# Performance work log

Measured on AMD Instinct MI355X. Metric: run time of the kernel, lower is better.

Reference implementation:

```python
import jax, jax.numpy as jnp
import numpy as np

N, M, C, IN, OUT = 65536, 512, 512, 256, 256
EPS = 1e-8


def setup_inputs() -> dict:
    key = jax.random.key(0)
    ks = jax.random.split(key, 12)
    d = {}
    d["x"] = jax.random.normal(ks[0], (1, IN), jnp.float32)
    d["memory"] = jax.random.normal(ks[1], (1, N, M), jnp.float32) * 0.05
    d["prev_read"] = jax.random.normal(ks[2], (1, M), jnp.float32) * 0.05
    d["h"] = jnp.ones((1, C), jnp.float32)
    d["c"] = jnp.ones((1, C), jnp.float32)
    d["read_state"] = jnp.zeros((1, N), jnp.float32)
    d["write_state"] = jnp.zeros((1, N), jnp.float32)
    d["W_ih"] = jax.random.normal(ks[3], (4 * C, IN + M), jnp.float32) * 0.02
    d["b_ih"] = jax.random.normal(ks[4], (4 * C,), jnp.float32) * 0.01
    d["W_hh"] = jax.random.normal(ks[5], (4 * C, C), jnp.float32) * 0.02
    d["b_hh"] = jax.random.normal(ks[6], (4 * C,), jnp.float32) * 0.01
    d["W_read"] = jax.random.normal(ks[7], (M + 6, C), jnp.float32) * 0.02
    d["b_read"] = jnp.zeros((M + 6,), jnp.float32)
    d["W_write"] = jax.random.normal(ks[8], (3 * M + 6, C), jnp.float32) * 0.02
    d["b_write"] = jnp.zeros((3 * M + 6,), jnp.float32)
    d["W_out"] = jax.random.normal(ks[9], (OUT, C + M), jnp.float32) * 0.02
    d["b_out"] = jnp.zeros((OUT,), jnp.float32)
    return d


def _address(head_out, w_prev, memory):
    # head_out: [B, M+6(+...)]; returns sharpened addressing weights [B, N]
    key_v = head_out[:, :M]
    beta = jax.nn.softplus(head_out[:, M:M + 1])          # [B,1]
    g = jax.nn.sigmoid(head_out[:, M + 1:M + 2])          # [B,1]
    shift = jax.nn.softmax(head_out[:, M + 2:M + 5], axis=1)  # [B,3]
    gamma = 1.0 + jax.nn.softplus(head_out[:, M + 5:M + 6])   # [B,1]
    # content addressing: cosine similarity over memory rows
    a = memory + EPS                                      # [B,N,M]
    b = key_v[:, None, :] + EPS                           # [B,1,M]
    dot = jnp.sum(a * b, axis=-1)                         # [B,N]
    na = jnp.maximum(jnp.sqrt(jnp.sum(a * a, axis=-1)), EPS)
    nb = jnp.maximum(jnp.sqrt(jnp.sum(b * b, axis=-1)), EPS)
    cos = dot / (na * nb)
    w_context = jax.nn.softmax(beta * cos, axis=1)        # [B,N]
    # NOTE: original code swaps args -> g gates the PREVIOUS weights
    w_interp = g * w_prev + (1.0 - g) * w_context
    # circular shift via 3-tap correlation (conv1d with circular pad)
    w_pad = jnp.concatenate([w_interp[:, -1:], w_interp, w_interp[:, :1]], axis=1)
    w_shift = (w_pad[:, :-2] * shift[:, 0:1]
               + w_pad[:, 1:-1] * shift[:, 1:2]
               + w_pad[:, 2:] * shift[:, 2:3])
    power = w_shift ** gamma
    return power / (jnp.sum(power, axis=1, keepdims=True) + EPS)


def reference(x, memory, prev_read, h, c, read_state, write_state,
              W_ih, b_ih, W_hh, b_hh, W_read, b_read, W_write, b_write,
              W_out, b_out):
    # LSTMCell controller (torch gate order: i, f, g, o)
    inp = jnp.concatenate([x, prev_read], axis=1)                   # [B, IN+M]
    gates = inp @ W_ih.T + b_ih + h @ W_hh.T + b_hh                 # [B, 4C]
    i_g, f_g, g_g, o_g = jnp.split(gates, 4, axis=1)
    c_new = jax.nn.sigmoid(f_g) * c + jax.nn.sigmoid(i_g) * jnp.tanh(g_g)
    h_new = jax.nn.sigmoid(o_g) * jnp.tanh(c_new)

    # read head
    r_out = h_new @ W_read.T + b_read
    w_r = _address(r_out, read_state, memory)                       # [B,N]
    # faithful to torch.matmul([B,N],[B,N,M]).sum(1): sums weights over batch
    read = jnp.einsum('n,bnm->bm', jnp.sum(w_r, axis=0), memory)    # [B,M]

    # write head
    w_out_head = h_new @ W_write.T + b_write
    w_w = _address(w_out_head, write_state, memory)                 # [B,N]
    erase = jax.nn.sigmoid(w_out_head[:, M + 6:2 * M + 6])          # [B,M]
    add = w_out_head[:, 2 * M + 6:3 * M + 6]                        # [B,M]
    memory_new = memory * (1.0 - w_w[:, :, None] * erase[:, None, :]) \
                 + w_w[:, :, None] * add[:, None, :]                # [B,N,M]

    out = jax.nn.sigmoid(jnp.concatenate([h_new, read], axis=1) @ W_out.T + b_out)
    del memory_new  # state update; torch forward returns only the output
    return out
```

## Files before the change

kernel.cpp:

```cpp
#include <hip/hip_runtime.h>
#include <math.h>

#define EPS 1e-8f
#define NN 65536
#define MAGIC 1.0f

#define WS_GATES 0
#define WS_HNEW  2048
#define WS_ROUT  2560
#define WS_PMAX  3104
#define WS_PEXP  5152
#define WS_S     7200
#define WS_PART  72992
#define WS_FLAGG 204064
#define WS_FLAGP 204192
#define WS_PART2 204448
#define WS_FLAG2 220832
#define WS_BF    262144
#define WS_PARTB 17039360
#define WS_PSUMB 18087936

typedef float f32x2 __attribute__((ext_vector_type(2)));

__device__ __forceinline__ float wave_sum(float v) {
    for (int o = 32; o > 0; o >>= 1) v += __shfl_xor(v, o);
    return v;
}
__device__ __forceinline__ float sigm(float x) { return 1.f / (1.f + expf(-x)); }
__device__ __forceinline__ float softplusf_(float x) {
    return x > 20.f ? x : log1pf(expf(x));
}
__device__ __forceinline__ float dot4(float4 a, float4 b) {
    return a.x * b.x + a.y * b.y + a.z * b.z + a.w * b.w;
}
__device__ __forceinline__ float4 ld4(const float* p) { return *(const float4*)p; }

__device__ __forceinline__ float ald(const float* p) {
    return __hip_atomic_load(p, __ATOMIC_RELAXED, __HIP_MEMORY_SCOPE_AGENT);
}
__device__ __forceinline__ void ast(float* p, float v) {
    __hip_atomic_store(p, v, __ATOMIC_RELAXED, __HIP_MEMORY_SCOPE_AGENT);
}
__device__ __forceinline__ void ast_rel(float* p, float v) {
    __hip_atomic_store(p, v, __ATOMIC_RELEASE, __HIP_MEMORY_SCOPE_AGENT);
}
__device__ __forceinline__ void acq_fence() {
    __builtin_amdgcn_fence(__ATOMIC_ACQUIRE, "agent");
}

__device__ __forceinline__ unsigned pk8(float4 v) {
    int u = __builtin_amdgcn_cvt_pk_fp8_f32(v.x, v.y, 0, false);
    u = __builtin_amdgcn_cvt_pk_fp8_f32(v.z, v.w, u, true);
    return (unsigned)u;
}

__global__ __launch_bounds__(256) void k_front(const float* __restrict__ x,
                                               const float* __restrict__ pr,
                                               const float* __restrict__ h,
                                               const float* __restrict__ c,
                                               const float* __restrict__ W_ih,
                                               const float* __restrict__ b_ih,
                                               const float* __restrict__ W_hh,
                                               const float* __restrict__ b_hh,
                                               const float* __restrict__ W_read,
                                               const float* __restrict__ b_read,
                                               float* __restrict__ ws) {
    const int b = blockIdx.x, t = threadIdx.x;
    const int lane = t & 63, wv = t >> 6;
    __shared__ float sh[512];

    if (b < 128) {
        #pragma unroll
        for (int i = 0; i < 4; ++i) {
            const int row = b * 16 + wv * 4 + i;
            const float* wi = W_ih + (size_t)row * 768;
            const float* wh = W_hh + (size_t)row * 512;
            float acc = dot4(ld4(wi + lane * 4), ld4(x + lane * 4))
                      + dot4(ld4(wi + 256 + lane * 4), ld4(pr + lane * 4))
                      + dot4(ld4(wi + 512 + lane * 4), ld4(pr + 256 + lane * 4))
                      + dot4(ld4(wh + lane * 4), ld4(h + lane * 4))
                      + dot4(ld4(wh + 256 + lane * 4), ld4(h + 256 + lane * 4));
            acc = wave_sum(acc);
            if (lane == 0) ast(ws + WS_GATES + row, acc + b_ih[row] + b_hh[row]);
        }
        __syncthreads();
        if (t == 0) ast_rel(ws + WS_FLAGG + b, MAGIC);
    }

    if (wv == 0) {
        int cap = 0;
        for (;;) {
            float v0 = ald(ws + WS_FLAGG + lane);
            float v1 = ald(ws + WS_FLAGG + 64 + lane);
            if (__all(v0 == MAGIC && v1 == MAGIC)) break;
            __builtin_amdgcn_s_sleep(1);
            if (++cap > (1 << 20)) break;
        }
        acq_fence();
    }
    __syncthreads();

    for (int j = t; j < 512; j += 256) {
        float ig = ald(ws + WS_GATES + j);
        float fg = ald(ws + WS_GATES + 512 + j);
        float gg = ald(ws + WS_GATES + 1024 + j);
        float og = ald(ws + WS_GATES + 1536 + j);
        float cn = sigm(fg) * c[j] + sigm(ig) * tanhf(gg);
        float hn = sigm(og) * tanhf(cn);
        sh[j] = hn;
        if (b == 0) ws[WS_HNEW + j] = hn;
    }
    __syncthreads();
    const int o = b * 4 + wv;
    if (o < 518) {
        const float* wr = W_read + (size_t)o * 512;
        float acc = dot4(ld4(wr + lane * 4), ld4(sh + lane * 4))
                  + dot4(ld4(wr + 256 + lane * 4), ld4(sh + 256 + lane * 4));
        acc = wave_sum(acc);
        if (lane == 0) ws[WS_ROUT + o] = acc + b_read[o];
    }
}

__global__ __launch_bounds__(256) void k_cos(const float* __restrict__ mem,
                                             float* __restrict__ ws) {
    const int t = threadIdx.x, lane = t & 63, wv = t >> 6;
    const int gw = blockIdx.x * 4 + wv;
    const float* key = ws + WS_ROUT;
    unsigned char* wsb = (unsigned char*)(ws + WS_BF);
    float4 ka = ld4(key + lane * 4);
    float4 kb = ld4(key + 256 + lane * 4);
    ka.x += EPS; ka.y += EPS; ka.z += EPS; ka.w += EPS;
    kb.x += EPS; kb.y += EPS; kb.z += EPS; kb.w += EPS;
    const float nb = fmaxf(__builtin_amdgcn_sqrtf(
                        wave_sum(dot4(ka, ka) + dot4(kb, kb))), EPS);
    const float beta = softplusf_(key[512]);
    float* sp = ws + WS_S;

    float4 va[4], vb[4], xa[4], xb[4];
    #pragma unroll
    for (int i = 0; i < 4; ++i) {
        const size_t n = (size_t)gw + i * 8192;
        va[i] = ld4(mem + n * 512 + lane * 4);
        vb[i] = ld4(mem + n * 512 + 256 + lane * 4);
    }
    #pragma unroll
    for (int i = 0; i < 4; ++i) {
        const size_t n = (size_t)gw + (4 + i) * 8192;
        xa[i] = ld4(mem + n * 512 + lane * 4);
        xb[i] = ld4(mem + n * 512 + 256 + lane * 4);
    }

    float m = -1e30f, e = 0.f;
    #pragma unroll
    for (int grp = 0; grp < 2; ++grp) {
        float d[4], q[4];
        #pragma unroll
        for (int i = 0; i < 4; ++i) {
            const size_t n = (size_t)gw + (grp * 4 + i) * 8192;
            *(unsigned*)(wsb + n * 512 + lane * 4) = pk8(va[i]);
            *(unsigned*)(wsb + n * 512 + 256 + lane * 4) = pk8(vb[i]);
            float4 wa = va[i], wb = vb[i];
            wa.x += EPS; wa.y += EPS; wa.z += EPS; wa.w += EPS;
            wb.x += EPS; wb.y += EPS; wb.z += EPS; wb.w += EPS;
            d[i] = dot4(wa, ka) + dot4(wb, kb);
            q[i] = dot4(wa, wa) + dot4(wb, wb);
        }
        if (grp == 0) {
            #pragma unroll
            for (int i = 0; i < 4; ++i) { va[i] = xa[i]; vb[i] = xb[i]; }
        }
        #pragma unroll
        for (int o = 32; o > 0; o >>= 1) {
            #pragma unroll
            for (int i = 0; i < 4; ++i) {
                d[i] += __shfl_xor(d[i], o);
                q[i] += __shfl_xor(q[i], o);
            }
        }
        float sv[4];
        #pragma unroll
        for (int i = 0; i < 4; ++i) {
            float na = fmaxf(__builtin_amdgcn_sqrtf(q[i]), EPS);
            sv[i] = beta * d[i] * __builtin_amdgcn_rcpf(na * nb);
        }
        float mysv = sv[0];
        if (lane == 1) mysv = sv[1];
        if (lane == 2) mysv = sv[2];
        if (lane == 3) mysv = sv[3];
        if (lane < 4) sp[gw + (grp * 4 + lane) * 8192] = mysv;
        float gm = fmaxf(fmaxf(sv[0], sv[1]), fmaxf(sv[2], sv[3]));
        float nm = fmaxf(m, gm);
        e = e * __expf(m - nm) + __expf(sv[0] - nm) + __expf(sv[1] - nm)
          + __expf(sv[2] - nm) + __expf(sv[3] - nm);
        m = nm;
    }

    __shared__ float sm[4], se[4];
    if (lane == 0) { sm[wv] = m; se[wv] = e; }
    __syncthreads();
    if (t == 0) {
        float M = fmaxf(fmaxf(sm[0], sm[1]), fmaxf(sm[2], sm[3]));
        float E = se[0] * __expf(sm[0] - M) + se[1] * __expf(sm[1] - M) +
                  se[2] * __expf(sm[2] - M) + se[3] * __expf(sm[3] - M);
        ws[WS_PMAX + blockIdx.x] = M;
        ws[WS_PEXP + blockIdx.x] = E;
    }
}

__global__ __launch_bounds__(256) void k_read(const float* __restrict__ rs,
                                              float* __restrict__ ws) {
    const int bb = blockIdx.x, t = threadIdx.x;
    const int lane = t & 63, wv = t >> 6;
    __shared__ float s_m[4], s_e[4];
    __shared__ float wi_l[34];
    __shared__ float pl[32];
    __shared__ float sacc[3][512];

    float m = -1e30f, e = 0.f;
    #pragma unroll
    for (int i = 0; i < 8; ++i) {
        float bm = ws[WS_PMAX + t + 256 * i], be = ws[WS_PEXP + t + 256 * i];
        float nm = fmaxf(m, bm);
        e = e * __expf(m - nm) + be * __expf(bm - nm);
        m = nm;
    }
    for (int o = 32; o > 0; o >>= 1) {
        float om = __shfl_xor(m, o), oe = __shfl_xor(e, o);
        float nm = fmaxf(m, om);
        e = e * __expf(m - nm) + oe * __expf(om - nm);
        m = nm;
    }
    if (lane == 0) { s_m[wv] = m; s_e[wv] = e; }
    __syncthreads();
    const float mx = fmaxf(fmaxf(s_m[0], s_m[1]), fmaxf(s_m[2], s_m[3]));
    const float Z = s_e[0] * __expf(s_m[0] - mx) + s_e[1] * __expf(s_m[1] - mx)
                  + s_e[2] * __expf(s_m[2] - mx) + s_e[3] * __expf(s_m[3] - mx);
    const float invZ = 1.f / Z;
    const float g = sigm(ws[WS_ROUT + 513]);
    float a3 = ws[WS_ROUT + 514], b3 = ws[WS_ROUT + 515], c3 = ws[WS_ROUT + 516];
    float mm = fmaxf(a3, fmaxf(b3, c3));
    float ea = __expf(a3 - mm), eb = __expf(b3 - mm), ec = __expf(c3 - mm);
    float ss = ea + eb + ec;
    const float s0 = ea / ss, s1 = eb / ss, s2 = ec / ss;
    const float gamma = 1.f + softplusf_(ws[WS_ROUT + 517]);

    const int start = bb * 32;
    if (t < 34) {
        int idx = (start - 1 + t) & (NN - 1);
        wi_l[t] = g * rs[idx] + (1.f - g) * __expf(ws[WS_S + idx] - mx) * invZ;
    }
    __syncthreads();
    float ps = 0.f;
    if (t < 32) {
        float wsh = wi_l[t] * s0 + wi_l[t + 1] * s1 + wi_l[t + 2] * s2;
        float pv = __powf(wsh, gamma);
        pl[t] = pv;
        ps = pv;
    }
    ps = wave_sum(ps);
    if (t == 0) ws[WS_PSUMB + bb] = ps;
    __syncthreads();

    const unsigned char* slab =
        (const unsigned char*)(ws + WS_BF) + (size_t)(start + wv * 8) * 512;
    float a0 = 0.f, a1 = 0.f, a2 = 0.f, a3f = 0.f,
          a4 = 0.f, a5 = 0.f, a6 = 0.f, a7 = 0.f;
    #pragma unroll
    for (int r = 0; r < 8; ++r) {
        float w = pl[wv * 8 + r];
        uint2 q = *(const uint2*)(slab + (size_t)r * 512 + lane * 8);
        f32x2 f0 = __builtin_amdgcn_cvt_pk_f32_fp8(q.x, false);
        f32x2 f1 = __builtin_amdgcn_cvt_pk_f32_fp8(q.x, true);
        f32x2 f2 = __builtin_amdgcn_cvt_pk_f32_fp8(q.y, false);
        f32x2 f3 = __builtin_amdgcn_cvt_pk_f32_fp8(q.y, true);
        a0 += w * f0.x;  a1 += w * f0.y;
        a2 += w * f1.x;  a3f += w * f1.y;
        a4 += w * f2.x;  a5 += w * f2.y;
        a6 += w * f3.x;  a7 += w * f3.y;
    }
    if (wv) {
        float* sw = sacc[wv - 1];
        sw[0 * 64 + lane] = a0; sw[1 * 64 + lane] = a1;
        sw[2 * 64 + lane] = a2; sw[3 * 64 + lane] = a3f;
        sw[4 * 64 + lane] = a4; sw[5 * 64 + lane] = a5;
        sw[6 * 64 + lane] = a6; sw[7 * 64 + lane] = a7;
    }
    __syncthreads();
    if (!wv) {
        #pragma unroll
        for (int i = 0; i < 3; ++i) {
            const float* sw = sacc[i];
            a0 += sw[0 * 64 + lane]; a1 += sw[1 * 64 + lane];
            a2 += sw[2 * 64 + lane]; a3f += sw[3 * 64 + lane];
            a4 += sw[4 * 64 + lane]; a5 += sw[5 * 64 + lane];
            a6 += sw[6 * 64 + lane]; a7 += sw[7 * 64 + lane];
        }
        float* pp = ws + WS_PARTB + (size_t)bb * 512 + lane * 8;
        *(float4*)pp = make_float4(a0, a1, a2, a3f);
        *(float4*)(pp + 4) = make_float4(a4, a5, a6, a7);
    }
}

__global__ __launch_bounds__(512) void k_out(const float* __restrict__ W_out,
                                             const float* __restrict__ b_out,
                                             float* __restrict__ ws,
                                             float* __restrict__ out) {
    const int b = blockIdx.x, t = threadIdx.x;
    const int lane = t & 63, wv = t >> 6;
    __shared__ float rd[512];
    __shared__ float s_z[8];

    {
        float s = 0.f;
        #pragma unroll
        for (int r = 0; r < 8; ++r)
            s += ws[WS_PARTB + (size_t)(8 * b + r) * 512 + t];
        ws[WS_PART + (size_t)b * 512 + t] = s;
    }
    __syncthreads();
    if (t == 0) ast_rel(ws + WS_FLAGP + b, MAGIC);
    if (b >= 32) return;

    if (wv == 0) {
        int cap = 0;
        for (;;) {
            float v0 = ald(ws + WS_FLAGP + lane);
            float v1 = ald(ws + WS_FLAGP + 64 + lane);
            float v2 = ald(ws + WS_FLAGP + 128 + lane);
            float v3 = ald(ws + WS_FLAGP + 192 + lane);
            if (__all(v0 == MAGIC && v1 == MAGIC && v2 == MAGIC && v3 == MAGIC))
                break;
            __builtin_amdgcn_s_sleep(1);
            if (++cap > (1 << 20)) break;
        }
        acq_fence();
    }
    __syncthreads();
    {
        float s = 0.f;
        #pragma unroll
        for (int r = 0; r < 8; ++r)
            s += ws[WS_PART + (size_t)(8 * b + r) * 512 + t];
        ws[WS_PART2 + (size_t)b * 512 + t] = s;
    }
    __syncthreads();
    if (t == 0) ast_rel(ws + WS_FLAG2 + b, MAGIC);
    if (wv == 0) {
        int cap = 0;
        for (;;) {
            float v = ald(ws + WS_FLAG2 + (lane & 31));
            if (__all(v == MAGIC)) break;
            __builtin_amdgcn_s_sleep(1);
            if (++cap > (1 << 20)) break;
        }
        acq_fence();
    }
    __syncthreads();
    float z = 0.f;
    #pragma unroll
    for (int i = 0; i < 4; ++i) z += ws[WS_PSUMB + t + 512 * i];
    z = wave_sum(z);
    if (lane == 0) s_z[wv] = z;
    __syncthreads();
    float Zp = 0.f;
    for (int i = 0; i < 8; ++i) Zp += s_z[i];
    const float invZp = 1.f / (Zp + EPS);
    {
        float s = 0.f;
        #pragma unroll
        for (int r = 0; r < 32; ++r)
            s += ws[WS_PART2 + (size_t)r * 512 + t];
        rd[t] = s * invZp;
    }
    __syncthreads();
    const int o = b * 8 + wv;
    const float* wo = W_out + (size_t)o * 1024;
    float a = dot4(ld4(wo + lane * 4), ld4(ws + WS_HNEW + lane * 4))
            + dot4(ld4(wo + 256 + lane * 4), ld4(ws + WS_HNEW + 256 + lane * 4))
            + dot4(ld4(wo + 512 + lane * 4), ld4(rd + lane * 4))
            + dot4(ld4(wo + 768 + lane * 4), ld4(rd + 256 + lane * 4));
    a = wave_sum(a);
    if (lane == 0) out[o] = sigm(a + b_out[o]);
}

extern "C" void kernel_launch(void* const* d_in, const int* in_sizes, int n_in,
                              void* d_out, int out_size, void* d_ws, size_t ws_size,
                              hipStream_t stream) {
    const float* x          = (const float*)d_in[0];
    const float* memory     = (const float*)d_in[1];
    const float* prev_read  = (const float*)d_in[2];
    const float* h          = (const float*)d_in[3];
    const float* c          = (const float*)d_in[4];
    const float* read_state = (const float*)d_in[5];
    const float* W_ih   = (const float*)d_in[7];
    const float* b_ih   = (const float*)d_in[8];
    const float* W_hh   = (const float*)d_in[9];
    const float* b_hh   = (const float*)d_in[10];
    const float* W_read = (const float*)d_in[11];
    const float* b_read = (const float*)d_in[12];
    const float* W_out  = (const float*)d_in[15];
    const float* b_out  = (const float*)d_in[16];
    float* ws  = (float*)d_ws;
    float* out = (float*)d_out;

    k_front<<<130, 256, 0, stream>>>(x, prev_read, h, c, W_ih, b_ih, W_hh, b_hh,
                                     W_read, b_read, ws);
    k_cos<<<2048, 256, 0, stream>>>(memory, ws);
    k_read<<<2048, 256, 0, stream>>>(read_state, ws);
    k_out<<<256, 512, 0, stream>>>(W_out, b_out, ws, out);
}
```

Measured before the change: 65.14 us.

## Fuse front LSTM/read-head kernel into cosine kernel with flag-based grid sync

Merges the front kernel (gates, LSTM cell, read-head projection) into the cosine-similarity kernel, launched as one 2048-block grid. The first 130 blocks do the front work and publish completion flags, and every block spins on those flags before the memory scan. This removes a kernel launch and its drain/fill gap. It also lets the memory loads be issued while earlier blocks finish. The cost is that the spin-wait relies on the first 130 blocks being scheduled and making progress, and the flags are never reset between calls.

```diff
diff --git a/kernel.cpp b/kernel.cpp
--- a/kernel.cpp
+++ b/kernel.cpp
@@ -16,6 +16,7 @@
 #define WS_FLAGP 204192
 #define WS_PART2 204448
 #define WS_FLAG2 220832
+#define WS_FLAGR 220864
 #define WS_BF    262144
 #define WS_PARTB 17039360
 #define WS_PSUMB 18087936
@@ -54,17 +55,18 @@
     return (unsigned)u;
 }
 
-__global__ __launch_bounds__(256) void k_front(const float* __restrict__ x,
-                                               const float* __restrict__ pr,
-                                               const float* __restrict__ h,
-                                               const float* __restrict__ c,
-                                               const float* __restrict__ W_ih,
-                                               const float* __restrict__ b_ih,
-                                               const float* __restrict__ W_hh,
-                                               const float* __restrict__ b_hh,
-                                               const float* __restrict__ W_read,
-                                               const float* __restrict__ b_read,
-                                               float* __restrict__ ws) {
+__global__ __launch_bounds__(256) void k_fc(const float* __restrict__ x,
+                                            const float* __restrict__ pr,
+                                            const float* __restrict__ h,
+                                            const float* __restrict__ c,
+                                            const float* __restrict__ W_ih,
+                                            const float* __restrict__ b_ih,
+                                            const float* __restrict__ W_hh,
+                                            const float* __restrict__ b_hh,
+                                            const float* __restrict__ W_read,
+                                            const float* __restrict__ b_read,
+                                            const float* __restrict__ mem,
+                                            float* __restrict__ ws) {
     const int b = blockIdx.x, t = threadIdx.x;
     const int lane = t & 63, wv = t >> 6;
     __shared__ float sh[512];
@@ -87,12 +89,49 @@
         if (t == 0) ast_rel(ws + WS_FLAGG + b, MAGIC);
     }
 
+    if (b < 130) {
+        if (wv == 0) {
+            int cap = 0;
+            for (;;) {
+                float v0 = ald(ws + WS_FLAGG + lane);
+                float v1 = ald(ws + WS_FLAGG + 64 + lane);
+                if (__all(v0 == MAGIC && v1 == MAGIC)) break;
+                __builtin_amdgcn_s_sleep(1);
+                if (++cap > (1 << 20)) break;
+            }
+            acq_fence();
+        }
+        __syncthreads();
+        for (int j = t; j < 512; j += 256) {
+            float ig = ald(ws + WS_GATES + j);
+            float fg = ald(ws + WS_GATES + 512 + j);
+            float gg = ald(ws + WS_GATES + 1024 + j);
+            float og = ald(ws + WS_GATES + 1536 + j);
+            float cn = sigm(fg) * c[j] + sigm(ig) * tanhf(gg);
+            float hn = sigm(og) * tanhf(cn);
+            sh[j] = hn;
+            if (b == 0) ws[WS_HNEW + j] = hn;
+        }
+        __syncthreads();
+        const int o = b * 4 + wv;
+        if (o < 518) {
+            const float* wr = W_read + (size_t)o * 512;
+            float acc = dot4(ld4(wr + lane * 4), ld4(sh + lane * 4))
+                      + dot4(ld4(wr + 256 + lane * 4), ld4(sh + 256 + lane * 4));
+            acc = wave_sum(acc);
+            if (lane == 0) ws[WS_ROUT + o] = acc + b_read[o];
+        }
+        __syncthreads();
+        if (t == 0) ast_rel(ws + WS_FLAGR + b, MAGIC);
+    }
+
     if (wv == 0) {
         int cap = 0;
         for (;;) {
-            float v0 = ald(ws + WS_FLAGG + lane);
-            float v1 = ald(ws + WS_FLAGG + 64 + lane);
-            if (__all(v0 == MAGIC && v1 == MAGIC)) break;
+            float v0 = ald(ws + WS_FLAGR + lane);
+            float v1 = ald(ws + WS_FLAGR + 64 + lane);
+            float v2 = ald(ws + WS_FLAGR + 128 + (lane & 1));
+            if (__all(v0 == MAGIC && v1 == MAGIC && v2 == MAGIC)) break;
             __builtin_amdgcn_s_sleep(1);
             if (++cap > (1 << 20)) break;
         }
@@ -100,31 +139,7 @@
     }
     __syncthreads();
 
-    for (int j = t; j < 512; j += 256) {
-        float ig = ald(ws + WS_GATES + j);
-        float fg = ald(ws + WS_GATES + 512 + j);
-        float gg = ald(ws + WS_GATES + 1024 + j);
-        float og = ald(ws + WS_GATES + 1536 + j);
-        float cn = sigm(fg) * c[j] + sigm(ig) * tanhf(gg);
-        float hn = sigm(og) * tanhf(cn);
-        sh[j] = hn;
-        if (b == 0) ws[WS_HNEW + j] = hn;
-    }
-    __syncthreads();
-    const int o = b * 4 + wv;
-    if (o < 518) {
-        const float* wr = W_read + (size_t)o * 512;
-        float acc = dot4(ld4(wr + lane * 4), ld4(sh + lane * 4))
-                  + dot4(ld4(wr + 256 + lane * 4), ld4(sh + 256 + lane * 4));
-        acc = wave_sum(acc);
-        if (lane == 0) ws[WS_ROUT + o] = acc + b_read[o];
-    }
-}
-
-__global__ __launch_bounds__(256) void k_cos(const float* __restrict__ mem,
-                                             float* __restrict__ ws) {
-    const int t = threadIdx.x, lane = t & 63, wv = t >> 6;
-    const int gw = blockIdx.x * 4 + wv;
+    const int gw = b * 4 + wv;
     const float* key = ws + WS_ROUT;
     unsigned char* wsb = (unsigned char*)(ws + WS_BF);
     float4 ka = ld4(key + lane * 4);
@@ -202,8 +217,8 @@
         float M = fmaxf(fmaxf(sm[0], sm[1]), fmaxf(sm[2], sm[3]));
         float E = se[0] * __expf(sm[0] - M) + se[1] * __expf(sm[1] - M) +
                   se[2] * __expf(sm[2] - M) + se[3] * __expf(sm[3] - M);
-        ws[WS_PMAX + blockIdx.x] = M;
-        ws[WS_PEXP + blockIdx.x] = E;
+        ws[WS_PMAX + b] = M;
+        ws[WS_PEXP + b] = E;
     }
 }
 
@@ -403,9 +418,8 @@
     float* ws  = (float*)d_ws;
     float* out = (float*)d_out;
 
-    k_front<<<130, 256, 0, stream>>>(x, prev_read, h, c, W_ih, b_ih, W_hh, b_hh,
-                                     W_read, b_read, ws);
-    k_cos<<<2048, 256, 0, stream>>>(memory, ws);
+    k_fc<<<2048, 256, 0, stream>>>(x, prev_read, h, c, W_ih, b_ih, W_hh, b_hh,
+                                   W_read, b_read, memory, ws);
     k_read<<<2048, 256, 0, stream>>>(read_state, ws);
     k_out<<<256, 512, 0, stream>>>(W_out, b_out, ws, out);
 }
```

Measured after the change: 77.33 us. 1.19x slower.
